# Kernel tuning notes

Hardware: AMD Instinct MI355X
Metric: run time of the kernel (lower is better)

Reference implementation:

```python
import jax, jax.numpy as jnp
import numpy as np

N = 50000   # nodes
E = 800000  # random edges (self loops added on top)
C = 64      # in = out channels per head
H = 4       # heads
NEG_SLOPE = 0.2  # PyG GATv2Conv default negative_slope


def setup_inputs() -> dict:
    key = jax.random.key(0)
    ks = jax.random.split(key, 6)
    s = 1.0 / np.sqrt(C)
    x = jax.random.normal(ks[0], (N, C), jnp.float32)
    network_edge = jax.random.randint(ks[1], (2, E), 0, N, dtype=jnp.int64)
    W_l = jax.random.normal(ks[2], (C, H * C), jnp.float32) * s
    b_l = jnp.zeros((H * C,), jnp.float32)
    W_r = jax.random.normal(ks[3], (C, H * C), jnp.float32) * s
    b_r = jnp.zeros((H * C,), jnp.float32)
    att = jax.random.normal(ks[4], (H, C), jnp.float32) * s
    bias = jnp.zeros((C,), jnp.float32)
    return {
        "x": x, "W_l": W_l, "b_l": b_l, "W_r": W_r, "b_r": b_r,
        "att": att, "bias": bias, "network_edge": network_edge,
        "batch_size": 1, "return_attention_weights": 0,
    }


def _gatv2_conv(x, W_l, b_l, W_r, b_r, att, bias, edge_index):
    n = x.shape[0]
    h, c = att.shape
    # add self loops (add_self_loops=True)
    self_idx = jnp.arange(n, dtype=edge_index.dtype)
    src = jnp.concatenate([edge_index[0], self_idx])  # message source j
    dst = jnp.concatenate([edge_index[1], self_idx])  # message target i
    # separate source/target projections (GATv2, share_weights=False)
    xl = (x @ W_l + b_l).reshape(n, h, c)
    xr = (x @ W_r + b_r).reshape(n, h, c)
    # per-edge GATv2 score: a^T LeakyReLU(x_l[j] + x_r[i])
    e = jax.nn.leaky_relu(xl[src] + xr[dst], NEG_SLOPE)  # [Etot,H,C]
    score = jnp.einsum('ehc,hc->eh', e, att)             # [Etot,H]
    # numerically-stable softmax over edges sharing the same target node
    smax = jax.ops.segment_max(score, dst, num_segments=n)  # [n,H]
    ex = jnp.exp(score - smax[dst])
    den = jax.ops.segment_sum(ex, dst, num_segments=n)
    alpha = ex / den[dst]  # dropout=0
    # weighted scatter-aggregate of source features
    out = jax.ops.segment_sum(alpha[:, :, None] * xl[src], dst, num_segments=n)
    out = out.mean(axis=1) + bias  # concat=False -> mean over heads, then bias
    return out, jnp.stack([src, dst]), alpha


def reference(x, W_l, b_l, W_r, b_r, att, bias, network_edge, batch_size,
              return_attention_weights):
    out, ei, alpha = _gatv2_conv(x, W_l, b_l, W_r, b_r, att, bias, network_edge)
    out = out.reshape(batch_size, -1, out.shape[-1])
    if return_attention_weights:
        return out, ei, alpha
    return out
```

## Files before the change

### kernel.cpp

```cpp
#include <hip/hip_runtime.h>

#define TM 16
#define SLACK 64

typedef float v2f __attribute__((ext_vector_type(2)));

__device__ __forceinline__ v2f unpack2(unsigned u) {
    union { unsigned u; float f; } lo, hi;
    lo.u = u << 16;
    hi.u = u & 0xffff0000u;
    v2f r;
    r.x = lo.f;
    r.y = hi.f;
    return r;
}
__device__ __forceinline__ unsigned short f2b(float f) {
    union { float f; unsigned u; } c;
    c.f = f;
    unsigned r = c.u + 0x7fffu + ((c.u >> 16) & 1u);
    return (unsigned short)(r >> 16);
}

__device__ __forceinline__ int edges_are_i64(const unsigned int* raw) {
    int f = 1;
#pragma unroll
    for (int k = 0; k < 16; ++k) f = f && (raw[2 * k + 1] == 0u);
    return f;
}
__device__ __forceinline__ int edge_at(const unsigned int* raw, int f,
                                       size_t idx) {
    return f ? (int)raw[2 * idx] : (int)raw[idx];
}

__global__ __launch_bounds__(256) void k_proj(
    const float* __restrict__ x, const float* __restrict__ Wl,
    const float* __restrict__ bl, const float* __restrict__ Wr,
    const float* __restrict__ br, unsigned short* __restrict__ xl,
    float* __restrict__ xr, int N,
    const unsigned int* __restrict__ eraw, int* __restrict__ deg, int E,
    int Etot, int* __restrict__ csrS, int* __restrict__ cursor) {
    __shared__ float xs[64][TM + 4];
    const int tid = threadIdx.x;
    const int base = blockIdx.x * TM;
    for (int t = tid; t < TM * 64; t += 256) {
        int m = t >> 6, k = t & 63;
        int n = base + m;
        xs[k][m] = (n < N) ? x[(size_t)n * 64 + k] : 0.f;
    }
    __syncthreads();
    const int j = tid;
    v2f accl2[TM / 2], accr2[TM / 2];
    const float blj = bl[j], brj = br[j];
#pragma unroll
    for (int m = 0; m < TM / 2; ++m) {
        accl2[m].x = blj; accl2[m].y = blj;
        accr2[m].x = brj; accr2[m].y = brj;
    }
    for (int k = 0; k < 64; ++k) {
        const float wl = Wl[(size_t)k * 256 + j];
        const float wr = Wr[(size_t)k * 256 + j];
        v2f wl2, wr2;
        wl2.x = wl; wl2.y = wl;
        wr2.x = wr; wr2.y = wr;
        const float4* xrow = (const float4*)(&xs[k][0]);
#pragma unroll
        for (int mm = 0; mm < TM / 4; ++mm) {
            float4 xv = xrow[mm];
            v2f x01, x23;
            x01.x = xv.x; x01.y = xv.y;
            x23.x = xv.z; x23.y = xv.w;
            accl2[2 * mm]     = __builtin_elementwise_fma(x01, wl2, accl2[2 * mm]);
            accl2[2 * mm + 1] = __builtin_elementwise_fma(x23, wl2, accl2[2 * mm + 1]);
            accr2[2 * mm]     = __builtin_elementwise_fma(x01, wr2, accr2[2 * mm]);
            accr2[2 * mm + 1] = __builtin_elementwise_fma(x23, wr2, accr2[2 * mm + 1]);
        }
    }
#pragma unroll
    for (int m = 0; m < TM; ++m) {
        int n = base + m;
        if (n < N) {
            float vl = (m & 1) ? accl2[m >> 1].y : accl2[m >> 1].x;
            float vr = (m & 1) ? accr2[m >> 1].y : accr2[m >> 1].x;
            xl[(size_t)n * 256 + j] = f2b(vl);
            xr[(size_t)n * 256 + j] = vr;
        }
    }
    const int stride = gridDim.x * 256;
    if (deg) {
        const int f = edges_are_i64(eraw);
        for (int e = blockIdx.x * 256 + tid; e < Etot; e += stride) {
            int d = (e < E) ? edge_at(eraw, f, (size_t)E + e) : (e - E);
            if ((unsigned)d >= (unsigned)N) d = 0;
            atomicAdd(&deg[d], 1);
        }
    }
    if (csrS) {
        const int f = edges_are_i64(eraw);
        for (int e = blockIdx.x * 256 + tid; e < Etot; e += stride) {
            int s, d;
            if (e < E) {
                s = edge_at(eraw, f, (size_t)e);
                d = edge_at(eraw, f, (size_t)E + e);
            } else {
                s = d = e - E;
            }
            if ((unsigned)s >= (unsigned)N) s = 0;
            if ((unsigned)d >= (unsigned)N) d = 0;
            int slot = atomicAdd(&cursor[d], 1);
            if (slot < SLACK) csrS[d * SLACK + slot] = s;
        }
    }
}

__global__ void k_scanA(const int* __restrict__ deg, int* __restrict__ bsum,
                        int N) {
    __shared__ int s[256];
    int t = threadIdx.x;
    int i = blockIdx.x * 256 + t;
    s[t] = (i < N) ? deg[i] : 0;
    __syncthreads();
    for (int d = 128; d > 0; d >>= 1) {
        if (t < d) s[t] += s[t + d];
        __syncthreads();
    }
    if (t == 0) bsum[blockIdx.x] = s[0];
}

__global__ void k_scanC(const int* __restrict__ deg,
                        const int* __restrict__ bsum,
                        int* __restrict__ row_start, int* __restrict__ cursor,
                        int Etot, int N) {
    __shared__ int s[256];
    __shared__ int off_s;
    const int t = threadIdx.x;
    s[t] = (t < blockIdx.x) ? bsum[t] : 0;
    __syncthreads();
    for (int d = 128; d > 0; d >>= 1) {
        if (t < d) s[t] += s[t + d];
        __syncthreads();
    }
    if (t == 0) off_s = s[0];
    __syncthreads();
    const int offset = off_s;
    __syncthreads();
    const int i = blockIdx.x * 256 + t;
    const int v = (i < N) ? deg[i] : 0;
    s[t] = v;
    __syncthreads();
    for (int d = 1; d < 256; d <<= 1) {
        int add = (t >= d) ? s[t - d] : 0;
        __syncthreads();
        s[t] += add;
        __syncthreads();
    }
    if (i < N) {
        int rs = s[t] - v + offset;
        row_start[i] = rs;
        cursor[i] = rs;
    }
    if (blockIdx.x == gridDim.x - 1 && t == 0) row_start[N] = Etot;
}

__global__ void k_scatter(const unsigned int* __restrict__ raw,
                          int* __restrict__ cursor, int* __restrict__ csr_src,
                          int E, int Etot, int N) {
    int e = blockIdx.x * 256 + threadIdx.x;
    if (e >= Etot) return;
    int f = edges_are_i64(raw);
    int s, d;
    if (e < E) {
        s = edge_at(raw, f, (size_t)e);
        d = edge_at(raw, f, (size_t)E + e);
    } else {
        s = d = e - E;
    }
    if ((unsigned)s >= (unsigned)N) s = 0;
    if ((unsigned)d >= (unsigned)N) d = 0;
    int slot = atomicAdd(&cursor[d], 1);
    if ((unsigned)slot < (unsigned)Etot) csr_src[slot] = s;
}

template <int ROWS>
__global__ __launch_bounds__(256) void k_aggregate_t(
    const unsigned short* __restrict__ xl, const float* __restrict__ xr,
    const float* __restrict__ att, const float* __restrict__ bias,
    const int* __restrict__ row_start, const int* __restrict__ csr_src,
    float* __restrict__ out, int N) {
    const int wave = threadIdx.x >> 6;
    const int lane = threadIdx.x & 63;
    const int i = blockIdx.x * 4 + wave;
    if (i >= N) return;
    const int half = lane >> 5;
    const int sl = lane & 31;
    const int co = sl * 8;

    v2f xrv[4], av[4];
    {
        const float4 x0 = *(const float4*)(xr + (size_t)i * 256 + co);
        const float4 x1 = *(const float4*)(xr + (size_t)i * 256 + co + 4);
        xrv[0].x = x0.x; xrv[0].y = x0.y;
        xrv[1].x = x0.z; xrv[1].y = x0.w;
        xrv[2].x = x1.x; xrv[2].y = x1.y;
        xrv[3].x = x1.z; xrv[3].y = x1.w;
        const float4 a0 = *(const float4*)(att + co);
        const float4 a1 = *(const float4*)(att + co + 4);
        av[0].x = a0.x; av[0].y = a0.y;
        av[1].x = a0.z; av[1].y = a0.w;
        av[2].x = a1.x; av[2].y = a1.y;
        av[3].x = a1.z; av[3].y = a1.w;
    }
    v2f accv[4];
#pragma unroll
    for (int p = 0; p < 4; ++p) { accv[p].x = 0.f; accv[p].y = 0.f; }
    float den = 0.f;
    int beg, end;
    if (ROWS == 0) {
        beg = row_start[i];
        end = row_start[i + 1];
    } else {
        int cnt = row_start[i];
        if (cnt > SLACK) cnt = SLACK;
        beg = i * SLACK;
        end = beg + cnt;
    }
    const int last = end - 1;
    const unsigned short* xlo = xl + co;

    constexpr int D = 3;
    uint4 cur[D];
    int sidx[D];
#pragma unroll
    for (int d = 0; d < D; ++d) {
        int s = csr_src[min(beg + 2 * d + half, last)];
        cur[d] = *(const uint4*)(xlo + (size_t)s * 256);
    }
#pragma unroll
    for (int d = 0; d < D; ++d)
        sidx[d] = csr_src[min(beg + 2 * D + 2 * d + half, last)];

    for (int e = beg; e < end; e += 2 * D) {
#pragma unroll
        for (int d = 0; d < D; ++d) {
            const uint4 cu = cur[d];
            cur[d] = *(const uint4*)(xlo + (size_t)sidx[d] * 256);
            sidx[d] = csr_src[min(e + 4 * D + 2 * d + half, last)];

            v2f c0 = unpack2(cu.x), c1 = unpack2(cu.y);
            v2f c2 = unpack2(cu.z), c3 = unpack2(cu.w);
            v2f v0 = c0 + xrv[0], v1 = c1 + xrv[1];
            v2f v2 = c2 + xrv[2], v3 = c3 + xrv[3];
            v0 = __builtin_elementwise_max(v0, v0 * 0.2f);
            v1 = __builtin_elementwise_max(v1, v1 * 0.2f);
            v2 = __builtin_elementwise_max(v2, v2 * 0.2f);
            v3 = __builtin_elementwise_max(v3, v3 * 0.2f);
            v2f t2a = av[0] * v0;
            v2f t2b = av[1] * v1;
            t2a = __builtin_elementwise_fma(av[2], v2, t2a);
            t2b = __builtin_elementwise_fma(av[3], v3, t2b);
            t2a += t2b;
            float t = t2a.x + t2a.y;
            t += __shfl_xor(t, 1);
            t += __shfl_xor(t, 2);
            t += __shfl_xor(t, 4);
            float w = __expf(fminf(t, 60.f));
            w = (e + 2 * d + half <= last) ? w : 0.f;
            den += w;
            v2f w2;
            w2.x = w; w2.y = w;
            accv[0] = __builtin_elementwise_fma(w2, c0, accv[0]);
            accv[1] = __builtin_elementwise_fma(w2, c1, accv[1]);
            accv[2] = __builtin_elementwise_fma(w2, c2, accv[2]);
            accv[3] = __builtin_elementwise_fma(w2, c3, accv[3]);
        }
    }
    den += __shfl_xor(den, 32);
    float r[8];
    r[0] = accv[0].x; r[1] = accv[0].y; r[2] = accv[1].x; r[3] = accv[1].y;
    r[4] = accv[2].x; r[5] = accv[2].y; r[6] = accv[3].x; r[7] = accv[3].y;
#pragma unroll
    for (int j = 0; j < 8; ++j) r[j] += __shfl_xor(r[j], 32);
    const float inv = 1.f / den;
#pragma unroll
    for (int j = 0; j < 8; ++j) r[j] *= inv;
#pragma unroll
    for (int j = 0; j < 8; ++j) {
        r[j] += __shfl_xor(r[j], 8);
        r[j] += __shfl_xor(r[j], 16);
    }
    if (lane < 8) {
        const float4 b0 = *(const float4*)(bias + lane * 8);
        const float4 b1 = *(const float4*)(bias + lane * 8 + 4);
        *(float4*)(out + (size_t)i * 64 + lane * 8) =
            make_float4(b0.x + 0.25f * r[0], b0.y + 0.25f * r[1],
                        b0.z + 0.25f * r[2], b0.w + 0.25f * r[3]);
        *(float4*)(out + (size_t)i * 64 + lane * 8 + 4) =
            make_float4(b1.x + 0.25f * r[4], b1.y + 0.25f * r[5],
                        b1.z + 0.25f * r[6], b1.w + 0.25f * r[7]);
    }
}

extern "C" void kernel_launch(void* const* d_in, const int* in_sizes, int n_in,
                              void* d_out, int out_size, void* d_ws,
                              size_t ws_size, hipStream_t stream) {
    const float* x    = (const float*)d_in[0];
    const float* Wl   = (const float*)d_in[1];
    const float* bl   = (const float*)d_in[2];
    const float* Wr   = (const float*)d_in[3];
    const float* br   = (const float*)d_in[4];
    const float* att  = (const float*)d_in[5];
    const float* bias = (const float*)d_in[6];
    const unsigned int* edges_raw = (const unsigned int*)d_in[7];

    const int N = in_sizes[0] / 64;
    const int E = in_sizes[7] / 2;
    const int Etot = E + N;

    char* p = (char*)d_ws;
    size_t off = 0;
    auto carve = [&](size_t bytes) -> char* {
        char* r = p + off;
        off = (off + bytes + 255) & ~(size_t)255;
        return r;
    };
    unsigned short* xl = (unsigned short*)carve((size_t)N * 256 * 2);
    float* xr = (float*)carve((size_t)N * 256 * 4);

    const size_t fast_need =
        off + ((((size_t)N * SLACK * 4) + 255) & ~(size_t)255) +
        (((size_t)N * 4 + 255) & ~(size_t)255) + 256;

    if (ws_size >= fast_need) {
        int* csrS   = (int*)carve((size_t)N * SLACK * 4);
        int* cursor = (int*)carve((size_t)N * 4);

        hipMemsetAsync(cursor, 0, (size_t)N * 4, stream);
        k_proj<<<(N + TM - 1) / TM, 256, 0, stream>>>(
            x, Wl, bl, Wr, br, xl, xr, N, edges_raw, nullptr, E, Etot,
            csrS, cursor);
        k_aggregate_t<1><<<(N + 3) / 4, 256, 0, stream>>>(
            xl, xr, att, bias, cursor, csrS, (float*)d_out, N);
    } else {
        int* csr_src   = (int*)carve((size_t)Etot * 4);
        int* row_start = (int*)carve((size_t)(N + 1) * 4);
        int* deg       = (int*)carve((size_t)N * 4);
        int* cursor    = (int*)carve((size_t)N * 4);
        int* bsum      = (int*)carve(1024 * 4);

        hipMemsetAsync(deg, 0, (size_t)N * 4, stream);
        k_proj<<<(N + TM - 1) / TM, 256, 0, stream>>>(
            x, Wl, bl, Wr, br, xl, xr, N, edges_raw, deg, E, Etot,
            nullptr, nullptr);
        const int NB = (N + 255) / 256;
        k_scanA<<<NB, 256, 0, stream>>>(deg, bsum, N);
        k_scanC<<<NB, 256, 0, stream>>>(deg, bsum, row_start, cursor, Etot, N);
        k_scatter<<<(Etot + 255) / 256, 256, 0, stream>>>(edges_raw, cursor,
                                                          csr_src, E, Etot, N);
        k_aggregate_t<0><<<(N + 3) / 4, 256, 0, stream>>>(
            xl, xr, att, bias, row_start, csr_src, (float*)d_out, N);
    }
}
```

Baseline: 210.1 us.

## Fuse memset, projection, CSR build and aggregation into one cooperative kernel

Replaces the memset, projection and aggregation launches on the fast path with a single cooperative persistent kernel. Grid-wide syncs separate the cursor reset, the projection plus edge bucketing, and the attention aggregation. This removes launch gaps and inter-kernel idle time. In exchange the grid is capped at occupancy-limited residency, so each block loops over many tiles and groups, and the grid barriers add their own sync cost.

Result: slower. 418.6 us (+99.3%).

```diff
diff --git a/kernel.cpp b/kernel.cpp
--- a/kernel.cpp
+++ b/kernel.cpp
@@ -1,4 +1,7 @@
 #include <hip/hip_runtime.h>
+#include <hip/hip_cooperative_groups.h>
+
+namespace cg = cooperative_groups;
 
 #define TM 16
 #define SLACK 64
@@ -20,7 +23,6 @@
     unsigned r = c.u + 0x7fffu + ((c.u >> 16) & 1u);
     return (unsigned short)(r >> 16);
 }
-
 __device__ __forceinline__ int edges_are_i64(const unsigned int* raw) {
     int f = 1;
 #pragma unroll
@@ -30,6 +32,194 @@
 __device__ __forceinline__ int edge_at(const unsigned int* raw, int f,
                                        size_t idx) {
     return f ? (int)raw[2 * idx] : (int)raw[idx];
+}
+
+__global__ __launch_bounds__(256) void k_fused(
+    const float* __restrict__ x, const float* __restrict__ Wl,
+    const float* __restrict__ bl, const float* __restrict__ Wr,
+    const float* __restrict__ br, const float* __restrict__ att,
+    const float* __restrict__ bias, unsigned short* __restrict__ xl,
+    float* __restrict__ xr, const unsigned int* __restrict__ eraw,
+    int* __restrict__ csrS, int* __restrict__ cursor, float* __restrict__ out,
+    int N, int E, int Etot, int ntiles, int ngroups) {
+    const int tid = threadIdx.x;
+    const int gstride = gridDim.x * 256;
+
+    for (int i = blockIdx.x * 256 + tid; i < N; i += gstride) cursor[i] = 0;
+    cg::this_grid().sync();
+
+    __shared__ float xs[64][TM + 4];
+    for (int tile = blockIdx.x; tile < ntiles; tile += gridDim.x) {
+        const int base = tile * TM;
+        __syncthreads();
+        for (int t = tid; t < TM * 64; t += 256) {
+            int m = t >> 6, k = t & 63;
+            int n = base + m;
+            xs[k][m] = (n < N) ? x[(size_t)n * 64 + k] : 0.f;
+        }
+        __syncthreads();
+        const int j = tid;
+        v2f accl2[TM / 2], accr2[TM / 2];
+        const float blj = bl[j], brj = br[j];
+#pragma unroll
+        for (int m = 0; m < TM / 2; ++m) {
+            accl2[m].x = blj; accl2[m].y = blj;
+            accr2[m].x = brj; accr2[m].y = brj;
+        }
+        for (int k = 0; k < 64; ++k) {
+            const float wl = Wl[(size_t)k * 256 + j];
+            const float wr = Wr[(size_t)k * 256 + j];
+            v2f wl2, wr2;
+            wl2.x = wl; wl2.y = wl;
+            wr2.x = wr; wr2.y = wr;
+            const float4* xrow = (const float4*)(&xs[k][0]);
+#pragma unroll
+            for (int mm = 0; mm < TM / 4; ++mm) {
+                float4 xv = xrow[mm];
+                v2f x01, x23;
+                x01.x = xv.x; x01.y = xv.y;
+                x23.x = xv.z; x23.y = xv.w;
+                accl2[2 * mm]     = __builtin_elementwise_fma(x01, wl2, accl2[2 * mm]);
+                accl2[2 * mm + 1] = __builtin_elementwise_fma(x23, wl2, accl2[2 * mm + 1]);
+                accr2[2 * mm]     = __builtin_elementwise_fma(x01, wr2, accr2[2 * mm]);
+                accr2[2 * mm + 1] = __builtin_elementwise_fma(x23, wr2, accr2[2 * mm + 1]);
+            }
+        }
+#pragma unroll
+        for (int m = 0; m < TM; ++m) {
+            int n = base + m;
+            if (n < N) {
+                float vl = (m & 1) ? accl2[m >> 1].y : accl2[m >> 1].x;
+                float vr = (m & 1) ? accr2[m >> 1].y : accr2[m >> 1].x;
+                xl[(size_t)n * 256 + j] = f2b(vl);
+                xr[(size_t)n * 256 + j] = vr;
+            }
+        }
+    }
+    {
+        const int f = edges_are_i64(eraw);
+        for (int e = blockIdx.x * 256 + tid; e < Etot; e += gstride) {
+            int s, d;
+            if (e < E) {
+                s = edge_at(eraw, f, (size_t)e);
+                d = edge_at(eraw, f, (size_t)E + e);
+            } else {
+                s = d = e - E;
+            }
+            if ((unsigned)s >= (unsigned)N) s = 0;
+            if ((unsigned)d >= (unsigned)N) d = 0;
+            int slot = atomicAdd(&cursor[d], 1);
+            if (slot < SLACK) csrS[d * SLACK + slot] = s;
+        }
+    }
+    cg::this_grid().sync();
+
+    const int wave = tid >> 6;
+    const int lane = tid & 63;
+    const int half = lane >> 5;
+    const int sl = lane & 31;
+    const int co = sl * 8;
+    for (int g = blockIdx.x; g < ngroups; g += gridDim.x) {
+        const int i = g * 4 + wave;
+        if (i >= N) continue;
+        v2f xrv[4], av[4];
+        {
+            const float4 x0 = *(const float4*)(xr + (size_t)i * 256 + co);
+            const float4 x1 = *(const float4*)(xr + (size_t)i * 256 + co + 4);
+            xrv[0].x = x0.x; xrv[0].y = x0.y;
+            xrv[1].x = x0.z; xrv[1].y = x0.w;
+            xrv[2].x = x1.x; xrv[2].y = x1.y;
+            xrv[3].x = x1.z; xrv[3].y = x1.w;
+            const float4 a0 = *(const float4*)(att + co);
+            const float4 a1 = *(const float4*)(att + co + 4);
+            av[0].x = a0.x; av[0].y = a0.y;
+            av[1].x = a0.z; av[1].y = a0.w;
+            av[2].x = a1.x; av[2].y = a1.y;
+            av[3].x = a1.z; av[3].y = a1.w;
+        }
+        v2f accv[4];
+#pragma unroll
+        for (int p = 0; p < 4; ++p) { accv[p].x = 0.f; accv[p].y = 0.f; }
+        float den = 0.f;
+        int cnt = cursor[i];
+        if (cnt > SLACK) cnt = SLACK;
+        const int beg = i * SLACK;
+        const int end = beg + cnt;
+        const int last = end - 1;
+        const unsigned short* xlo = xl + co;
+
+        constexpr int D = 3;
+        uint4 cur[D];
+        int sidx[D];
+#pragma unroll
+        for (int d = 0; d < D; ++d) {
+            int s = csrS[min(beg + 2 * d + half, last)];
+            cur[d] = *(const uint4*)(xlo + (size_t)s * 256);
+        }
+#pragma unroll
+        for (int d = 0; d < D; ++d)
+            sidx[d] = csrS[min(beg + 2 * D + 2 * d + half, last)];
+
+        for (int e = beg; e < end; e += 2 * D) {
+#pragma unroll
+            for (int d = 0; d < D; ++d) {
+                const uint4 cu = cur[d];
+                cur[d] = *(const uint4*)(xlo + (size_t)sidx[d] * 256);
+                sidx[d] = csrS[min(e + 4 * D + 2 * d + half, last)];
+
+                v2f c0 = unpack2(cu.x), c1 = unpack2(cu.y);
+                v2f c2 = unpack2(cu.z), c3 = unpack2(cu.w);
+                v2f v0 = c0 + xrv[0], v1 = c1 + xrv[1];
+                v2f v2 = c2 + xrv[2], v3 = c3 + xrv[3];
+                v0 = __builtin_elementwise_max(v0, v0 * 0.2f);
+                v1 = __builtin_elementwise_max(v1, v1 * 0.2f);
+                v2 = __builtin_elementwise_max(v2, v2 * 0.2f);
+                v3 = __builtin_elementwise_max(v3, v3 * 0.2f);
+                v2f t2a = av[0] * v0;
+                v2f t2b = av[1] * v1;
+                t2a = __builtin_elementwise_fma(av[2], v2, t2a);
+                t2b = __builtin_elementwise_fma(av[3], v3, t2b);
+                t2a += t2b;
+                float t = t2a.x + t2a.y;
+                t += __shfl_xor(t, 1);
+                t += __shfl_xor(t, 2);
+                t += __shfl_xor(t, 4);
+                float w = __expf(fminf(t, 60.f));
+                w = (e + 2 * d + half <= last) ? w : 0.f;
+                den += w;
+                v2f w2;
+                w2.x = w; w2.y = w;
+                accv[0] = __builtin_elementwise_fma(w2, c0, accv[0]);
+                accv[1] = __builtin_elementwise_fma(w2, c1, accv[1]);
+                accv[2] = __builtin_elementwise_fma(w2, c2, accv[2]);
+                accv[3] = __builtin_elementwise_fma(w2, c3, accv[3]);
+            }
+        }
+        den += __shfl_xor(den, 32);
+        float r[8];
+        r[0] = accv[0].x; r[1] = accv[0].y; r[2] = accv[1].x; r[3] = accv[1].y;
+        r[4] = accv[2].x; r[5] = accv[2].y; r[6] = accv[3].x; r[7] = accv[3].y;
+#pragma unroll
+        for (int j = 0; j < 8; ++j) r[j] += __shfl_xor(r[j], 32);
+        const float inv = 1.f / den;
+#pragma unroll
+        for (int j = 0; j < 8; ++j) r[j] *= inv;
+#pragma unroll
+        for (int j = 0; j < 8; ++j) {
+            r[j] += __shfl_xor(r[j], 8);
+            r[j] += __shfl_xor(r[j], 16);
+        }
+        if (lane < 8) {
+            const float4 b0 = *(const float4*)(bias + lane * 8);
+            const float4 b1 = *(const float4*)(bias + lane * 8 + 4);
+            *(float4*)(out + (size_t)i * 64 + lane * 8) =
+                make_float4(b0.x + 0.25f * r[0], b0.y + 0.25f * r[1],
+                            b0.z + 0.25f * r[2], b0.w + 0.25f * r[3]);
+            *(float4*)(out + (size_t)i * 64 + lane * 8 + 4) =
+                make_float4(b1.x + 0.25f * r[4], b1.y + 0.25f * r[5],
+                            b1.z + 0.25f * r[6], b1.w + 0.25f * r[7]);
+        }
+    }
 }
 
 __global__ __launch_bounds__(256) void k_proj(
@@ -332,13 +522,59 @@
     if (ws_size >= fast_need) {
         int* csrS   = (int*)carve((size_t)N * SLACK * 4);
         int* cursor = (int*)carve((size_t)N * 4);
-
-        hipMemsetAsync(cursor, 0, (size_t)N * 4, stream);
-        k_proj<<<(N + TM - 1) / TM, 256, 0, stream>>>(
-            x, Wl, bl, Wr, br, xl, xr, N, edges_raw, nullptr, E, Etot,
-            csrS, cursor);
-        k_aggregate_t<1><<<(N + 3) / 4, 256, 0, stream>>>(
-            xl, xr, att, bias, cursor, csrS, (float*)d_out, N);
+        int ntiles  = (N + TM - 1) / TM;
+        int ngroups = (N + 3) / 4;
+
+        static int coop_grid = -2;
+        if (coop_grid == -2) {
+            int nb = 0, ncu = 0;
+            hipDeviceProp_t props;
+            if (hipGetDeviceProperties(&props, 0) == hipSuccess)
+                ncu = props.multiProcessorCount;
+            if (ncu > 0 &&
+                hipOccupancyMaxActiveBlocksPerMultiprocessor(
+                    &nb, (const void*)k_fused, 256, 0) == hipSuccess &&
+                nb > 0)
+                coop_grid = nb * ncu;
+            else
+                coop_grid = -1;
+        }
+
+        bool coop_done = false;
+        if (coop_grid > 0) {
+            const float* a_x = x; const float* a_Wl = Wl;
+            const float* a_bl = bl; const float* a_Wr = Wr;
+            const float* a_br = br; const float* a_att = att;
+            const float* a_bias = bias;
+            unsigned short* a_xl = xl; float* a_xr = xr;
+            const unsigned int* a_eraw = edges_raw;
+            int* a_csrS = csrS; int* a_cursor = cursor;
+            float* a_out = (float*)d_out;
+            int a_N = N, a_E = E, a_Etot = Etot;
+            int a_ntiles = ntiles, a_ngroups = ngroups;
+            void* args[] = {(void*)&a_x,      (void*)&a_Wl,
+                            (void*)&a_bl,     (void*)&a_Wr,
+                            (void*)&a_br,     (void*)&a_att,
+                            (void*)&a_bias,   (void*)&a_xl,
+                            (void*)&a_xr,     (void*)&a_eraw,
+                            (void*)&a_csrS,   (void*)&a_cursor,
+                            (void*)&a_out,    (void*)&a_N,
+                            (void*)&a_E,      (void*)&a_Etot,
+                            (void*)&a_ntiles, (void*)&a_ngroups};
+            hipError_t err = hipLaunchCooperativeKernel(
+                (const void*)k_fused, dim3(coop_grid), dim3(256), args, 0,
+                stream);
+            coop_done = (err == hipSuccess);
+            if (!coop_done) coop_grid = -1;
+        }
+        if (!coop_done) {
+            (void)hipMemsetAsync(cursor, 0, (size_t)N * 4, stream);
+            k_proj<<<ntiles, 256, 0, stream>>>(x, Wl, bl, Wr, br, xl, xr, N,
+                                               edges_raw, nullptr, E,
+                                               Etot, csrS, cursor);
+            k_aggregate_t<1><<<ngroups, 256, 0, stream>>>(
+                xl, xr, att, bias, cursor, csrS, (float*)d_out, N);
+        }
     } else {
         int* csr_src   = (int*)carve((size_t)Etot * 4);
         int* row_start = (int*)carve((size_t)(N + 1) * 4);
@@ -346,7 +582,7 @@
         int* cursor    = (int*)carve((size_t)N * 4);
         int* bsum      = (int*)carve(1024 * 4);
 
-        hipMemsetAsync(deg, 0, (size_t)N * 4, stream);
+        (void)hipMemsetAsync(deg, 0, (size_t)N * 4, stream);
         k_proj<<<(N + TM - 1) / TM, 256, 0, stream>>>(
             x, Wl, bl, Wr, br, xl, xr, N, edges_raw, deg, E, Etot,
             nullptr, nullptr);
```
